# Performance work log

Hardware: AMD Instinct MI355X
Metric: run time of the kernel (lower is better)

Reference implementation:

```python
import jax, jax.numpy as jnp
import numpy as np

D_MODEL, D_K, D_V, H, M = 512, 64, 64, 8, 40
LN_EPS = 1e-3  # keras LayerNormalization default epsilon


def setup_inputs() -> dict:
    key = jax.random.key(0)
    ks = jax.random.split(key, 12)
    b, nq, nk = 16, 1024, 1024
    s = 1.0 / np.sqrt(D_MODEL)
    return {
        "queries": jax.random.normal(ks[0], (b, nq, D_MODEL), jnp.float32),
        "keys": jax.random.normal(ks[1], (b, nk, D_MODEL), jnp.float32),
        "values": jax.random.normal(ks[2], (b, nk, D_MODEL), jnp.float32),
        "attention_weights": jax.random.uniform(ks[3], (b, 1, nq, nk), jnp.float32),
        "Wq": jax.random.normal(ks[4], (D_MODEL, H * D_K), jnp.float32) * s,
        "bq": jnp.zeros((H * D_K,), jnp.float32),
        "Wk": jax.random.normal(ks[5], (D_MODEL, H * D_K), jnp.float32) * s,
        "bk": jnp.zeros((H * D_K,), jnp.float32),
        "Wv": jax.random.normal(ks[6], (D_MODEL, H * D_V), jnp.float32) * s,
        "bv": jnp.zeros((H * D_V,), jnp.float32),
        "Wo": jax.random.normal(ks[7], (H * D_V, D_MODEL), jnp.float32) * (1.0 / np.sqrt(H * D_V)),
        "bo": jnp.zeros((D_MODEL,), jnp.float32),
        "memK": jax.random.normal(ks[8], (1, M, H * D_K), jnp.float32) * (1.0 / D_K),
        "memV": jax.random.normal(ks[9], (1, M, H * D_V), jnp.float32) * (1.0 / M),
        "gamma": jnp.ones((D_MODEL,), jnp.float32),
        "beta": jnp.zeros((D_MODEL,), jnp.float32),
    }


def reference(queries, keys, values, attention_weights, Wq, bq, Wk, bk, Wv, bv,
              Wo, bo, memK, memV, gamma, beta):
    b, nq, _ = queries.shape
    nk = keys.shape[1]
    # scaled learned memory slots
    mem_k = np.sqrt(D_K).astype(np.float32) * memK      # [1, M, H*D_K]
    mem_v = np.sqrt(M).astype(np.float32) * memV        # [1, M, H*D_V]
    # projections
    q = (queries @ Wq + bq).reshape(b, nq, H, D_K).transpose(0, 2, 1, 3)   # [b,h,nq,dk]
    k_proj = keys @ Wk + bk                                                # [b,nk,H*D_K]
    v_proj = values @ Wv + bv                                              # [b,nk,H*D_V]
    k_cat = jnp.concatenate([k_proj, jnp.broadcast_to(mem_k, (b, M, H * D_K))], axis=1)
    v_cat = jnp.concatenate([v_proj, jnp.broadcast_to(mem_v, (b, M, H * D_V))], axis=1)
    k = k_cat.reshape(b, nk + M, H, D_K).transpose(0, 2, 1, 3)             # [b,h,nk+m,dk]
    v = v_cat.reshape(b, nk + M, H, D_V).transpose(0, 2, 1, 3)             # [b,h,nk+m,dv]
    att = jnp.einsum('bhqd,bhkd->bhqk', q, k) / np.sqrt(D_K).astype(np.float32)
    # only the non-memory columns are modulated by attention_weights
    att = jnp.concatenate([att[..., :nk] * attention_weights, att[..., nk:]], axis=-1)
    att = jax.nn.softmax(att, axis=-1)
    out = jnp.einsum('bhqk,bhkd->bhqd', att, v).transpose(0, 2, 1, 3).reshape(b, nq, H * D_V)
    out = out @ Wo + bo  # dropout is identity at inference
    # residual + LayerNorm (keras eps=1e-3)
    x = queries + out
    mu = jnp.mean(x, axis=-1, keepdims=True)
    var = jnp.mean((x - mu) ** 2, axis=-1, keepdims=True)
    return gamma * (x - mu) * jax.lax.rsqrt(var + LN_EPS) + beta
```

## Files before the change

### kernel.cpp

```cpp
#include <hip/hip_runtime.h>
#include <hip/hip_bf16.h>
#include <math.h>

typedef __attribute__((ext_vector_type(8))) short bf16x8;
typedef __attribute__((ext_vector_type(4))) short s16x4;
typedef __attribute__((ext_vector_type(4))) float f32x4;

static __device__ __forceinline__ short f2bf(float f) {
    union { float f; unsigned u; } v; v.f = f;
    unsigned r = v.u + 0x7FFFu + ((v.u >> 16) & 1u);
    return (short)(r >> 16);
}

__global__ __launch_bounds__(256) void wt_kernel(
    const float* __restrict__ Wq, const float* __restrict__ Wk,
    const float* __restrict__ Wv, const float* __restrict__ Wo,
    short* __restrict__ WqT, short* __restrict__ WkT,
    short* __restrict__ WvT, short* __restrict__ WoT)
{
    __shared__ short lds[64][65];
    const float* src; short* dst;
    if (blockIdx.z == 0)      { src = Wq; dst = WqT; }
    else if (blockIdx.z == 1) { src = Wk; dst = WkT; }
    else if (blockIdx.z == 2) { src = Wv; dst = WvT; }
    else                      { src = Wo; dst = WoT; }
    const int kb = blockIdx.x * 64, nb = blockIdx.y * 64;
    const int t = threadIdx.x;
    const int c = t & 63, r0 = t >> 6;
#pragma unroll
    for (int rr = 0; rr < 16; ++rr) {
        const int r = r0 * 16 + rr;
        lds[c][r] = f2bf(src[(size_t)(kb + r) * 512 + nb + c]);
    }
    __syncthreads();
#pragma unroll
    for (int rr = 0; rr < 16; ++rr) {
        const int n = r0 * 16 + rr;
        dst[(size_t)(nb + n) * 512 + kb + c] = lds[n][c];
    }
}

__global__ __launch_bounds__(256) void mem_kernel(
    const float* __restrict__ memK, const float* __restrict__ memV,
    short* __restrict__ Kb, short* __restrict__ VbT)
{
    const int idx = blockIdx.x * 256 + threadIdx.x;
    if (idx >= 16 * 8 * 40 * 64) return;
    const int d = idx & 63;
    const int m = (idx >> 6) % 40;
    const int h = (idx / 2560) & 7;
    const int b = idx / 20480;
    const int src = m * 512 + h * 64 + d;
    const int bh = b * 8 + h;
    Kb[((size_t)bh * 1064 + 1024 + m) * 64 + d] = f2bf(8.0f * memK[src]);
    VbT[((size_t)bh * 64 + d) * 1088 + 1024 + m] = f2bf(sqrtf(40.0f) * memV[src]);
}

__global__ __launch_bounds__(256) void proj_gemm(
    const float* __restrict__ A, const short* __restrict__ BT,
    const float* __restrict__ bias, short* __restrict__ out, int OUTROWS, int vmode)
{
    __shared__ short As[128][40];
    __shared__ short Bs[128][40];
    const int t = threadIdx.x;
    const int lane = t & 63, w = t >> 6;
    const int wr = w >> 1, wc = w & 1;
    const int l16 = lane & 15, g4 = lane >> 4;
    const int m0 = blockIdx.y * 128, n0 = blockIdx.x * 128;

    f32x4 acc[4][4];
#pragma unroll
    for (int i = 0; i < 4; ++i)
#pragma unroll
        for (int j = 0; j < 4; ++j) acc[i][j] = (f32x4){0.f, 0.f, 0.f, 0.f};

    const int sar = t >> 3, sak = (t & 7) * 4;
    const int sbr = t >> 2, sbk = (t & 3) * 8;

    for (int kt = 0; kt < 16; ++kt) {
        const int k0 = kt * 32;
#pragma unroll
        for (int rr = 0; rr < 4; ++rr) {
            const int row = sar + rr * 32;
            const float4 v = *reinterpret_cast<const float4*>(&A[(size_t)(m0 + row) * 512 + k0 + sak]);
            s16x4 bv; bv.x = f2bf(v.x); bv.y = f2bf(v.y); bv.z = f2bf(v.z); bv.w = f2bf(v.w);
            *reinterpret_cast<s16x4*>(&As[row][sak]) = bv;
        }
#pragma unroll
        for (int nn = 0; nn < 2; ++nn) {
            const int nrow = sbr + nn * 64;
            *reinterpret_cast<bf16x8*>(&Bs[nrow][sbk]) =
                *reinterpret_cast<const bf16x8*>(&BT[(size_t)(n0 + nrow) * 512 + k0 + sbk]);
        }
        __syncthreads();
        bf16x8 af[4], bfr[4];
#pragma unroll
        for (int mi = 0; mi < 4; ++mi)
            af[mi] = *reinterpret_cast<const bf16x8*>(&As[wr * 64 + mi * 16 + l16][g4 * 8]);
#pragma unroll
        for (int ni = 0; ni < 4; ++ni)
            bfr[ni] = *reinterpret_cast<const bf16x8*>(&Bs[wc * 64 + ni * 16 + l16][g4 * 8]);
#pragma unroll
        for (int mi = 0; mi < 4; ++mi)
#pragma unroll
            for (int ni = 0; ni < 4; ++ni)
                acc[mi][ni] = __builtin_amdgcn_mfma_f32_16x16x32_bf16(af[mi], bfr[ni], acc[mi][ni], 0, 0, 0);
        __syncthreads();
    }
#pragma unroll
    for (int mi = 0; mi < 4; ++mi) {
#pragma unroll
        for (int ni = 0; ni < 4; ++ni) {
            const int col = n0 + wc * 64 + ni * 16 + l16;
            const int h = col >> 6, d = col & 63;
            const float bb = bias[col];
#pragma unroll
            for (int r = 0; r < 4; ++r) {
                const int rowg = m0 + wr * 64 + mi * 16 + g4 * 4 + r;
                const int b = rowg >> 10, nn = rowg & 1023;
                const short val = f2bf(acc[mi][ni][r] + bb);
                if (vmode)
                    out[(((size_t)b * 8 + h) * 64 + d) * 1088 + nn] = val;
                else
                    out[(((size_t)b * 8 + h) * OUTROWS + nn) * 64 + d] = val;
            }
        }
    }
}

__global__ __launch_bounds__(256) void attn_kernel(
    const short* __restrict__ Qb, const short* __restrict__ Kb,
    const short* __restrict__ VbT, const float* __restrict__ aw,
    short* __restrict__ AO)
{
    __shared__ short Ks[64][72];
    __shared__ short Vs[64][72];
    __shared__ short Ps[4][16][72];

    const int n = blockIdx.x;
    const int xcd = n & 7, s_ = n >> 3, j = s_ & 7, gh = s_ >> 3;
    const int g = gh * 8 + xcd;
    const int h = j, qt = g & 15, b = g >> 4;
    const int bh = b * 8 + h;
    const int t = threadIdx.x;
    const int lane = t & 63, w = t >> 6;
    const int l16 = lane & 15, g4 = lane >> 4;
    const int qrow0 = qt * 64 + w * 16;

    bf16x8 qf0, qf1;
    {
        const short* qp = Qb + ((size_t)bh * 1024 + qrow0 + l16) * 64 + g4 * 8;
        qf0 = *reinterpret_cast<const bf16x8*>(qp);
        qf1 = *reinterpret_cast<const bf16x8*>(qp + 32);
    }

    f32x4 O[4];
#pragma unroll
    for (int i = 0; i < 4; ++i) O[i] = (f32x4){0.f, 0.f, 0.f, 0.f};
    float m_r[4] = {-1e30f, -1e30f, -1e30f, -1e30f};
    float l_r[4] = {0.f, 0.f, 0.f, 0.f};

    const int str = t >> 2;
    const int stc = (t & 3) * 16;

    for (int kt = 0; kt < 17; ++kt) {
        const int kb = kt * 64;
        const bool useaw = (kb < 1024);
        float awv[4][4];
        if (useaw) {
#pragma unroll
            for (int r = 0; r < 4; ++r) {
                const size_t awbase = ((size_t)b * 1024 + qrow0 + g4 * 4 + r) * 1024 + kb + l16;
#pragma unroll
                for (int sub = 0; sub < 4; ++sub)
                    awv[r][sub] = aw[awbase + sub * 16];
            }
        }
        {
            const int rg = kb + str;
            bf16x8 k0 = {0,0,0,0,0,0,0,0}, k1 = {0,0,0,0,0,0,0,0};
            if (rg < 1064) {
                const short* kp = &Kb[((size_t)bh * 1064 + rg) * 64 + stc];
                k0 = *reinterpret_cast<const bf16x8*>(kp);
                k1 = *reinterpret_cast<const bf16x8*>(kp + 8);
            }
            *reinterpret_cast<bf16x8*>(&Ks[str][stc]) = k0;
            *reinterpret_cast<bf16x8*>(&Ks[str][stc + 8]) = k1;
        }
        {
            const short* vp = &VbT[((size_t)bh * 64 + str) * 1088 + kb + stc];
            bf16x8 v0 = {0,0,0,0,0,0,0,0}, v1 = {0,0,0,0,0,0,0,0};
            if (kb + stc + 8 <= 1064)  v0 = *reinterpret_cast<const bf16x8*>(vp);
            if (kb + stc + 16 <= 1064) v1 = *reinterpret_cast<const bf16x8*>(vp + 8);
            *reinterpret_cast<bf16x8*>(&Vs[str][stc]) = v0;
            *reinterpret_cast<bf16x8*>(&Vs[str][stc + 8]) = v1;
        }
        __syncthreads();

        f32x4 S[4];
        __builtin_amdgcn_s_setprio(1);
#pragma unroll
        for (int sub = 0; sub < 4; ++sub) {
            bf16x8 kf0 = *reinterpret_cast<const bf16x8*>(&Ks[sub * 16 + l16][g4 * 8]);
            bf16x8 kf1 = *reinterpret_cast<const bf16x8*>(&Ks[sub * 16 + l16][32 + g4 * 8]);
            f32x4 z = {0.f, 0.f, 0.f, 0.f};
            z = __builtin_amdgcn_mfma_f32_16x16x32_bf16(qf0, kf0, z, 0, 0, 0);
            S[sub] = __builtin_amdgcn_mfma_f32_16x16x32_bf16(qf1, kf1, z, 0, 0, 0);
        }
        __builtin_amdgcn_s_setprio(0);

        const bool tail = (kb + 64 > 1064);
        float corr[4], pv[4][4];
#pragma unroll
        for (int r = 0; r < 4; ++r) {
            float sv[4];
#pragma unroll
            for (int sub = 0; sub < 4; ++sub) {
                float x = S[sub][r] * 0.125f;
                if (useaw) x *= awv[r][sub];
                if (tail && (kb + sub * 16 + l16 >= 1064)) x = -1e30f;
                sv[sub] = x;
            }
            float mx = fmaxf(fmaxf(sv[0], sv[1]), fmaxf(sv[2], sv[3]));
#pragma unroll
            for (int off = 1; off < 16; off <<= 1)
                mx = fmaxf(mx, __shfl_xor(mx, off));
            const float mn = fmaxf(m_r[r], mx);
            corr[r] = __expf(m_r[r] - mn);
            m_r[r] = mn;
            float rs = 0.f;
#pragma unroll
            for (int sub = 0; sub < 4; ++sub) {
                pv[r][sub] = __expf(sv[sub] - mn);
                rs += pv[r][sub];
            }
#pragma unroll
            for (int off = 1; off < 16; off <<= 1)
                rs += __shfl_xor(rs, off);
            l_r[r] = l_r[r] * corr[r] + rs;
        }
#pragma unroll
        for (int r = 0; r < 4; ++r)
#pragma unroll
            for (int sub = 0; sub < 4; ++sub)
                Ps[w][g4 * 4 + r][sub * 16 + l16] = f2bf(pv[r][sub]);
#pragma unroll
        for (int i = 0; i < 4; ++i)
#pragma unroll
            for (int r = 0; r < 4; ++r)
                O[i][r] *= corr[r];
        bf16x8 pf0 = *reinterpret_cast<const bf16x8*>(&Ps[w][l16][g4 * 8]);
        bf16x8 pf1 = *reinterpret_cast<const bf16x8*>(&Ps[w][l16][32 + g4 * 8]);
        __builtin_amdgcn_s_setprio(1);
#pragma unroll
        for (int sub = 0; sub < 4; ++sub) {
            bf16x8 vf0 = *reinterpret_cast<const bf16x8*>(&Vs[sub * 16 + l16][g4 * 8]);
            bf16x8 vf1 = *reinterpret_cast<const bf16x8*>(&Vs[sub * 16 + l16][32 + g4 * 8]);
            O[sub] = __builtin_amdgcn_mfma_f32_16x16x32_bf16(pf0, vf0, O[sub], 0, 0, 0);
            O[sub] = __builtin_amdgcn_mfma_f32_16x16x32_bf16(pf1, vf1, O[sub], 0, 0, 0);
        }
        __builtin_amdgcn_s_setprio(0);
        __syncthreads();
    }
#pragma unroll
    for (int r = 0; r < 4; ++r) {
        const float inv = 1.0f / l_r[r];
        const int qg = qrow0 + g4 * 4 + r;
        const size_t base = ((size_t)b * 1024 + qg) * 512 + h * 64;
#pragma unroll
        for (int sub = 0; sub < 4; ++sub)
            AO[base + sub * 16 + l16] = f2bf(O[sub][r] * inv);
    }
}

__global__ __launch_bounds__(256) void out_gemm(
    const short* __restrict__ A, const short* __restrict__ BT,
    const float* __restrict__ bias, const float* __restrict__ resid,
    float* __restrict__ out)
{
    __shared__ short As[128][40];
    __shared__ short Bs[128][40];
    const int t = threadIdx.x;
    const int lane = t & 63, w = t >> 6;
    const int wr = w >> 1, wc = w & 1;
    const int l16 = lane & 15, g4 = lane >> 4;
    const int m0 = blockIdx.y * 128, n0 = blockIdx.x * 128;

    f32x4 acc[4][4];
#pragma unroll
    for (int i = 0; i < 4; ++i)
#pragma unroll
        for (int j = 0; j < 4; ++j) acc[i][j] = (f32x4){0.f, 0.f, 0.f, 0.f};

    const int sr = t >> 2, sk = (t & 3) * 8;

    for (int kt = 0; kt < 16; ++kt) {
        const int k0 = kt * 32;
#pragma unroll
        for (int nn = 0; nn < 2; ++nn) {
            const int row = sr + nn * 64;
            *reinterpret_cast<bf16x8*>(&As[row][sk]) =
                *reinterpret_cast<const bf16x8*>(&A[(size_t)(m0 + row) * 512 + k0 + sk]);
            *reinterpret_cast<bf16x8*>(&Bs[row][sk]) =
                *reinterpret_cast<const bf16x8*>(&BT[(size_t)(n0 + row) * 512 + k0 + sk]);
        }
        __syncthreads();
        bf16x8 af[4], bfr[4];
#pragma unroll
        for (int mi = 0; mi < 4; ++mi)
            af[mi] = *reinterpret_cast<const bf16x8*>(&As[wr * 64 + mi * 16 + l16][g4 * 8]);
#pragma unroll
        for (int ni = 0; ni < 4; ++ni)
            bfr[ni] = *reinterpret_cast<const bf16x8*>(&Bs[wc * 64 + ni * 16 + l16][g4 * 8]);
#pragma unroll
        for (int mi = 0; mi < 4; ++mi)
#pragma unroll
            for (int ni = 0; ni < 4; ++ni)
                acc[mi][ni] = __builtin_amdgcn_mfma_f32_16x16x32_bf16(af[mi], bfr[ni], acc[mi][ni], 0, 0, 0);
        __syncthreads();
    }
#pragma unroll
    for (int mi = 0; mi < 4; ++mi) {
#pragma unroll
        for (int ni = 0; ni < 4; ++ni) {
            const int col = n0 + wc * 64 + ni * 16 + l16;
            const float bb = bias[col];
#pragma unroll
            for (int r = 0; r < 4; ++r) {
                const int rowg = m0 + wr * 64 + mi * 16 + g4 * 4 + r;
                out[(size_t)rowg * 512 + col] = acc[mi][ni][r] + bb + resid[(size_t)rowg * 512 + col];
            }
        }
    }
}

__global__ __launch_bounds__(256) void ln_kernel(
    float* __restrict__ x, const float* __restrict__ gamma, const float* __restrict__ beta)
{
    const int row = blockIdx.x * 4 + (threadIdx.x >> 6);
    const int lane = threadIdx.x & 63;
    float* rp = x + (size_t)row * 512;
    const float4 v0 = *reinterpret_cast<const float4*>(&rp[lane * 4]);
    const float4 v1 = *reinterpret_cast<const float4*>(&rp[256 + lane * 4]);
    float s = v0.x + v0.y + v0.z + v0.w + v1.x + v1.y + v1.z + v1.w;
    float sq = v0.x * v0.x + v0.y * v0.y + v0.z * v0.z + v0.w * v0.w
             + v1.x * v1.x + v1.y * v1.y + v1.z * v1.z + v1.w * v1.w;
#pragma unroll
    for (int off = 1; off < 64; off <<= 1) {
        s += __shfl_xor(s, off);
        sq += __shfl_xor(sq, off);
    }
    const float mu = s * (1.f / 512.f);
    const float var = sq * (1.f / 512.f) - mu * mu;
    const float inv = rsqrtf(var + 1e-3f);
    const float4 g0 = *reinterpret_cast<const float4*>(&gamma[lane * 4]);
    const float4 g1 = *reinterpret_cast<const float4*>(&gamma[256 + lane * 4]);
    const float4 b0 = *reinterpret_cast<const float4*>(&beta[lane * 4]);
    const float4 b1 = *reinterpret_cast<const float4*>(&beta[256 + lane * 4]);
    float4 o0, o1;
    o0.x = (v0.x - mu) * inv * g0.x + b0.x;
    o0.y = (v0.y - mu) * inv * g0.y + b0.y;
    o0.z = (v0.z - mu) * inv * g0.z + b0.z;
    o0.w = (v0.w - mu) * inv * g0.w + b0.w;
    o1.x = (v1.x - mu) * inv * g1.x + b1.x;
    o1.y = (v1.y - mu) * inv * g1.y + b1.y;
    o1.z = (v1.z - mu) * inv * g1.z + b1.z;
    o1.w = (v1.w - mu) * inv * g1.w + b1.w;
    *reinterpret_cast<float4*>(&rp[lane * 4]) = o0;
    *reinterpret_cast<float4*>(&rp[256 + lane * 4]) = o1;
}

extern "C" void kernel_launch(void* const* d_in, const int* in_sizes, int n_in,
                              void* d_out, int out_size, void* d_ws, size_t ws_size,
                              hipStream_t stream) {
    const float* queries = (const float*)d_in[0];
    const float* keys    = (const float*)d_in[1];
    const float* values  = (const float*)d_in[2];
    const float* aw      = (const float*)d_in[3];
    const float* Wq = (const float*)d_in[4];
    const float* bq = (const float*)d_in[5];
    const float* Wk = (const float*)d_in[6];
    const float* bk = (const float*)d_in[7];
    const float* Wv = (const float*)d_in[8];
    const float* bv = (const float*)d_in[9];
    const float* Wo = (const float*)d_in[10];
    const float* bo = (const float*)d_in[11];
    const float* memK = (const float*)d_in[12];
    const float* memV = (const float*)d_in[13];
    const float* gamma = (const float*)d_in[14];
    const float* beta  = (const float*)d_in[15];
    float* out = (float*)d_out;

    char* ws = (char*)d_ws;
    short* WqT = (short*)(ws + 0);
    short* WkT = (short*)(ws + 524288);
    short* WvT = (short*)(ws + 1048576);
    short* WoT = (short*)(ws + 1572864);
    short* Qb  = (short*)(ws + 2097152);
    short* Kb  = (short*)(ws + 2097152 + 16777216);
    short* VbT = (short*)(ws + 2097152 + 16777216 + 17432576);
    short* AO  = (short*)(ws + 2097152 + 16777216 + 17432576 + 17825792);

    wt_kernel<<<dim3(8, 8, 4), 256, 0, stream>>>(Wq, Wk, Wv, Wo, WqT, WkT, WvT, WoT);
    mem_kernel<<<dim3(1280), 256, 0, stream>>>(memK, memV, Kb, VbT);
    proj_gemm<<<dim3(4, 128), 256, 0, stream>>>(queries, WqT, bq, Qb, 1024, 0);
    proj_gemm<<<dim3(4, 128), 256, 0, stream>>>(keys, WkT, bk, Kb, 1064, 0);
    proj_gemm<<<dim3(4, 128), 256, 0, stream>>>(values, WvT, bv, VbT, 1064, 1);
    attn_kernel<<<dim3(2048), 256, 0, stream>>>(Qb, Kb, VbT, aw, AO);
    out_gemm<<<dim3(4, 128), 256, 0, stream>>>(AO, WoT, bo, queries, out);
    ln_kernel<<<dim3(4096), 256, 0, stream>>>(out, gamma, beta);
}
```

Baseline: 419.0 us.

## Use direct global-to-LDS loads with swizzle in GEMMs and lazy softmax rescaling

The projection and output GEMMs now stage tiles with global_load_lds 16-byte copies into XOR-swizzled LDS, use a 64x128 tile with K-step 64, and double the grid. The projection GEMM keeps fp32 A in LDS and converts to bf16 when building fragments. The attention softmax skips rescaling O and l unless some row max grows by more than 8, and writes P to LDS inside the exp loop. This targets staging overhead, register pressure, bank conflicts and per-tile rescale work, at the cost of a larger fp32 LDS footprint and a threshold-based rescale that allows somewhat larger exponent values.

New measurement: 435.6 us. 1.04x slower.

```diff
diff --git a/kernel.cpp b/kernel.cpp
--- a/kernel.cpp
+++ b/kernel.cpp
@@ -11,6 +11,10 @@
     unsigned r = v.u + 0x7FFFu + ((v.u >> 16) & 1u);
     return (short)(r >> 16);
 }
+
+#define GL2LDS16(g, s) __builtin_amdgcn_global_load_lds( \
+    (const __attribute__((address_space(1))) void*)(g),  \
+    (__attribute__((address_space(3))) void*)(s), 16, 0, 0)
 
 __global__ __launch_bounds__(256) void wt_kernel(
     const float* __restrict__ Wq, const float* __restrict__ Wk,
@@ -60,55 +64,75 @@
     const float* __restrict__ A, const short* __restrict__ BT,
     const float* __restrict__ bias, short* __restrict__ out, int OUTROWS, int vmode)
 {
-    __shared__ short As[128][40];
-    __shared__ short Bs[128][40];
+    __shared__ float As[4096];
+    __shared__ short Bs[8192];
     const int t = threadIdx.x;
     const int lane = t & 63, w = t >> 6;
     const int wr = w >> 1, wc = w & 1;
     const int l16 = lane & 15, g4 = lane >> 4;
-    const int m0 = blockIdx.y * 128, n0 = blockIdx.x * 128;
-
-    f32x4 acc[4][4];
-#pragma unroll
-    for (int i = 0; i < 4; ++i)
+    const int m0 = blockIdx.y * 64, n0 = blockIdx.x * 128;
+
+    f32x4 acc[2][4];
+#pragma unroll
+    for (int i = 0; i < 2; ++i)
 #pragma unroll
         for (int j = 0; j < 4; ++j) acc[i][j] = (f32x4){0.f, 0.f, 0.f, 0.f};
 
-    const int sar = t >> 3, sak = (t & 7) * 4;
-    const int sbr = t >> 2, sbk = (t & 3) * 8;
-
-    for (int kt = 0; kt < 16; ++kt) {
-        const int k0 = kt * 32;
-#pragma unroll
-        for (int rr = 0; rr < 4; ++rr) {
-            const int row = sar + rr * 32;
-            const float4 v = *reinterpret_cast<const float4*>(&A[(size_t)(m0 + row) * 512 + k0 + sak]);
-            s16x4 bv; bv.x = f2bf(v.x); bv.y = f2bf(v.y); bv.z = f2bf(v.z); bv.w = f2bf(v.w);
-            *reinterpret_cast<s16x4*>(&As[row][sak]) = bv;
-        }
-#pragma unroll
-        for (int nn = 0; nn < 2; ++nn) {
-            const int nrow = sbr + nn * 64;
-            *reinterpret_cast<bf16x8*>(&Bs[nrow][sbk]) =
-                *reinterpret_cast<const bf16x8*>(&BT[(size_t)(n0 + nrow) * 512 + k0 + sbk]);
-        }
-        __syncthreads();
-        bf16x8 af[4], bfr[4];
-#pragma unroll
-        for (int mi = 0; mi < 4; ++mi)
-            af[mi] = *reinterpret_cast<const bf16x8*>(&As[wr * 64 + mi * 16 + l16][g4 * 8]);
-#pragma unroll
-        for (int ni = 0; ni < 4; ++ni)
-            bfr[ni] = *reinterpret_cast<const bf16x8*>(&Bs[wc * 64 + ni * 16 + l16][g4 * 8]);
-#pragma unroll
-        for (int mi = 0; mi < 4; ++mi)
-#pragma unroll
-            for (int ni = 0; ni < 4; ++ni)
-                acc[mi][ni] = __builtin_amdgcn_mfma_f32_16x16x32_bf16(af[mi], bfr[ni], acc[mi][ni], 0, 0, 0);
-        __syncthreads();
-    }
-#pragma unroll
-    for (int mi = 0; mi < 4; ++mi) {
+    int arow_[4], acol_[4], brow_[4], bcol_[4];
+#pragma unroll
+    for (int c = 0; c < 4; ++c) {
+        const int chunk = c * 4 + w;
+        const int ar = chunk * 4 + (lane >> 4);
+        const int alb = ((lane & 15) * 16) ^ ((ar & 7) << 4);
+        arow_[c] = ar; acol_[c] = alb >> 2;
+        const int br = chunk * 8 + (lane >> 3);
+        const int blb = ((lane & 7) * 16) ^ ((br & 7) << 4);
+        brow_[c] = br; bcol_[c] = blb >> 1;
+    }
+
+    for (int kt = 0; kt < 8; ++kt) {
+        const int k0 = kt * 64;
+#pragma unroll
+        for (int c = 0; c < 4; ++c) {
+            GL2LDS16(&A[(size_t)(m0 + arow_[c]) * 512 + k0 + acol_[c]],
+                     &As[(c * 4 + w) * 256 + lane * 4]);
+            GL2LDS16(&BT[(size_t)(n0 + brow_[c]) * 512 + k0 + bcol_[c]],
+                     &Bs[(c * 4 + w) * 512 + lane * 8]);
+        }
+        __syncthreads();
+#pragma unroll
+        for (int kk = 0; kk < 2; ++kk) {
+            bf16x8 af[2], bfr[4];
+#pragma unroll
+            for (int mi = 0; mi < 2; ++mi) {
+                const int ar = wr * 32 + mi * 16 + l16;
+                const int lb0 = (kk * 128 + g4 * 32) ^ ((ar & 7) << 4);
+                const float4 f0 = *reinterpret_cast<const float4*>(
+                    reinterpret_cast<const char*>(As) + ar * 256 + lb0);
+                const float4 f1 = *reinterpret_cast<const float4*>(
+                    reinterpret_cast<const char*>(As) + ar * 256 + (lb0 ^ 16));
+                bf16x8 a;
+                a[0] = f2bf(f0.x); a[1] = f2bf(f0.y); a[2] = f2bf(f0.z); a[3] = f2bf(f0.w);
+                a[4] = f2bf(f1.x); a[5] = f2bf(f1.y); a[6] = f2bf(f1.z); a[7] = f2bf(f1.w);
+                af[mi] = a;
+            }
+#pragma unroll
+            for (int ni = 0; ni < 4; ++ni) {
+                const int br = wc * 64 + ni * 16 + l16;
+                const int lb = (kk * 64 + g4 * 16) ^ ((br & 7) << 4);
+                bfr[ni] = *reinterpret_cast<const bf16x8*>(
+                    reinterpret_cast<const char*>(Bs) + br * 128 + lb);
+            }
+#pragma unroll
+            for (int mi = 0; mi < 2; ++mi)
+#pragma unroll
+                for (int ni = 0; ni < 4; ++ni)
+                    acc[mi][ni] = __builtin_amdgcn_mfma_f32_16x16x32_bf16(af[mi], bfr[ni], acc[mi][ni], 0, 0, 0);
+        }
+        __syncthreads();
+    }
+#pragma unroll
+    for (int mi = 0; mi < 2; ++mi) {
 #pragma unroll
         for (int ni = 0; ni < 4; ++ni) {
             const int col = n0 + wc * 64 + ni * 16 + l16;
@@ -116,7 +140,7 @@
             const float bb = bias[col];
 #pragma unroll
             for (int r = 0; r < 4; ++r) {
-                const int rowg = m0 + wr * 64 + mi * 16 + g4 * 4 + r;
+                const int rowg = m0 + wr * 32 + mi * 16 + g4 * 4 + r;
                 const int b = rowg >> 10, nn = rowg & 1023;
                 const short val = f2bf(acc[mi][ni][r] + bb);
                 if (vmode)
@@ -210,45 +234,50 @@
         __builtin_amdgcn_s_setprio(0);
 
         const bool tail = (kb + 64 > 1064);
-        float corr[4], pv[4][4];
+        float sv[4][4], mx[4];
 #pragma unroll
         for (int r = 0; r < 4; ++r) {
-            float sv[4];
 #pragma unroll
             for (int sub = 0; sub < 4; ++sub) {
                 float x = S[sub][r] * 0.125f;
                 if (useaw) x *= awv[r][sub];
                 if (tail && (kb + sub * 16 + l16 >= 1064)) x = -1e30f;
-                sv[sub] = x;
-            }
-            float mx = fmaxf(fmaxf(sv[0], sv[1]), fmaxf(sv[2], sv[3]));
+                sv[r][sub] = x;
+            }
+            float m2 = fmaxf(fmaxf(sv[r][0], sv[r][1]), fmaxf(sv[r][2], sv[r][3]));
 #pragma unroll
             for (int off = 1; off < 16; off <<= 1)
-                mx = fmaxf(mx, __shfl_xor(mx, off));
-            const float mn = fmaxf(m_r[r], mx);
-            corr[r] = __expf(m_r[r] - mn);
-            m_r[r] = mn;
+                m2 = fmaxf(m2, __shfl_xor(m2, off));
+            mx[r] = m2;
+        }
+        bool grew = false;
+#pragma unroll
+        for (int r = 0; r < 4; ++r) grew = grew || (mx[r] > m_r[r] + 8.0f);
+        if (__any(grew)) {
+#pragma unroll
+            for (int r = 0; r < 4; ++r) {
+                const float mn = fmaxf(m_r[r], mx[r]);
+                const float corr = __expf(m_r[r] - mn);
+                m_r[r] = mn;
+                l_r[r] *= corr;
+#pragma unroll
+                for (int i = 0; i < 4; ++i) O[i][r] *= corr;
+            }
+        }
+#pragma unroll
+        for (int r = 0; r < 4; ++r) {
             float rs = 0.f;
 #pragma unroll
             for (int sub = 0; sub < 4; ++sub) {
-                pv[r][sub] = __expf(sv[sub] - mn);
-                rs += pv[r][sub];
+                const float p = __expf(sv[r][sub] - m_r[r]);
+                rs += p;
+                Ps[w][g4 * 4 + r][sub * 16 + l16] = f2bf(p);
             }
 #pragma unroll
             for (int off = 1; off < 16; off <<= 1)
                 rs += __shfl_xor(rs, off);
-            l_r[r] = l_r[r] * corr[r] + rs;
-        }
-#pragma unroll
-        for (int r = 0; r < 4; ++r)
-#pragma unroll
-            for (int sub = 0; sub < 4; ++sub)
-                Ps[w][g4 * 4 + r][sub * 16 + l16] = f2bf(pv[r][sub]);
-#pragma unroll
-        for (int i = 0; i < 4; ++i)
-#pragma unroll
-            for (int r = 0; r < 4; ++r)
-                O[i][r] *= corr[r];
+            l_r[r] += rs;
+        }
         bf16x8 pf0 = *reinterpret_cast<const bf16x8*>(&Ps[w][l16][g4 * 8]);
         bf16x8 pf1 = *reinterpret_cast<const bf16x8*>(&Ps[w][l16][32 + g4 * 8]);
         __builtin_amdgcn_s_setprio(1);
@@ -278,56 +307,81 @@
     const float* __restrict__ bias, const float* __restrict__ resid,
     float* __restrict__ out)
 {
-    __shared__ short As[128][40];
-    __shared__ short Bs[128][40];
+    __shared__ short Asb[4096];
+    __shared__ short Bs[8192];
     const int t = threadIdx.x;
     const int lane = t & 63, w = t >> 6;
     const int wr = w >> 1, wc = w & 1;
     const int l16 = lane & 15, g4 = lane >> 4;
-    const int m0 = blockIdx.y * 128, n0 = blockIdx.x * 128;
-
-    f32x4 acc[4][4];
-#pragma unroll
-    for (int i = 0; i < 4; ++i)
+    const int m0 = blockIdx.y * 64, n0 = blockIdx.x * 128;
+
+    f32x4 acc[2][4];
+#pragma unroll
+    for (int i = 0; i < 2; ++i)
 #pragma unroll
         for (int j = 0; j < 4; ++j) acc[i][j] = (f32x4){0.f, 0.f, 0.f, 0.f};
 
-    const int sr = t >> 2, sk = (t & 3) * 8;
-
-    for (int kt = 0; kt < 16; ++kt) {
-        const int k0 = kt * 32;
-#pragma unroll
-        for (int nn = 0; nn < 2; ++nn) {
-            const int row = sr + nn * 64;
-            *reinterpret_cast<bf16x8*>(&As[row][sk]) =
-                *reinterpret_cast<const bf16x8*>(&A[(size_t)(m0 + row) * 512 + k0 + sk]);
-            *reinterpret_cast<bf16x8*>(&Bs[row][sk]) =
-                *reinterpret_cast<const bf16x8*>(&BT[(size_t)(n0 + row) * 512 + k0 + sk]);
-        }
-        __syncthreads();
-        bf16x8 af[4], bfr[4];
-#pragma unroll
-        for (int mi = 0; mi < 4; ++mi)
-            af[mi] = *reinterpret_cast<const bf16x8*>(&As[wr * 64 + mi * 16 + l16][g4 * 8]);
-#pragma unroll
-        for (int ni = 0; ni < 4; ++ni)
-            bfr[ni] = *reinterpret_cast<const bf16x8*>(&Bs[wc * 64 + ni * 16 + l16][g4 * 8]);
-#pragma unroll
-        for (int mi = 0; mi < 4; ++mi)
-#pragma unroll
-            for (int ni = 0; ni < 4; ++ni)
-                acc[mi][ni] = __builtin_amdgcn_mfma_f32_16x16x32_bf16(af[mi], bfr[ni], acc[mi][ni], 0, 0, 0);
-        __syncthreads();
-    }
-#pragma unroll
-    for (int mi = 0; mi < 4; ++mi) {
+    int arow_[2], acol_[2], brow_[4], bcol_[4];
+#pragma unroll
+    for (int c = 0; c < 2; ++c) {
+        const int chunk = c * 4 + w;
+        const int ar = chunk * 8 + (lane >> 3);
+        const int alb = ((lane & 7) * 16) ^ ((ar & 7) << 4);
+        arow_[c] = ar; acol_[c] = alb >> 1;
+    }
+#pragma unroll
+    for (int c = 0; c < 4; ++c) {
+        const int chunk = c * 4 + w;
+        const int br = chunk * 8 + (lane >> 3);
+        const int blb = ((lane & 7) * 16) ^ ((br & 7) << 4);
+        brow_[c] = br; bcol_[c] = blb >> 1;
+    }
+
+    for (int kt = 0; kt < 8; ++kt) {
+        const int k0 = kt * 64;
+#pragma unroll
+        for (int c = 0; c < 2; ++c)
+            GL2LDS16(&A[(size_t)(m0 + arow_[c]) * 512 + k0 + acol_[c]],
+                     &Asb[(c * 4 + w) * 512 + lane * 8]);
+#pragma unroll
+        for (int c = 0; c < 4; ++c)
+            GL2LDS16(&BT[(size_t)(n0 + brow_[c]) * 512 + k0 + bcol_[c]],
+                     &Bs[(c * 4 + w) * 512 + lane * 8]);
+        __syncthreads();
+#pragma unroll
+        for (int kk = 0; kk < 2; ++kk) {
+            bf16x8 af[2], bfr[4];
+#pragma unroll
+            for (int mi = 0; mi < 2; ++mi) {
+                const int ar = wr * 32 + mi * 16 + l16;
+                const int lb = (kk * 64 + g4 * 16) ^ ((ar & 7) << 4);
+                af[mi] = *reinterpret_cast<const bf16x8*>(
+                    reinterpret_cast<const char*>(Asb) + ar * 128 + lb);
+            }
+#pragma unroll
+            for (int ni = 0; ni < 4; ++ni) {
+                const int br = wc * 64 + ni * 16 + l16;
+                const int lb = (kk * 64 + g4 * 16) ^ ((br & 7) << 4);
+                bfr[ni] = *reinterpret_cast<const bf16x8*>(
+                    reinterpret_cast<const char*>(Bs) + br * 128 + lb);
+            }
+#pragma unroll
+            for (int mi = 0; mi < 2; ++mi)
+#pragma unroll
+                for (int ni = 0; ni < 4; ++ni)
+                    acc[mi][ni] = __builtin_amdgcn_mfma_f32_16x16x32_bf16(af[mi], bfr[ni], acc[mi][ni], 0, 0, 0);
+        }
+        __syncthreads();
+    }
+#pragma unroll
+    for (int mi = 0; mi < 2; ++mi) {
 #pragma unroll
         for (int ni = 0; ni < 4; ++ni) {
             const int col = n0 + wc * 64 + ni * 16 + l16;
             const float bb = bias[col];
 #pragma unroll
             for (int r = 0; r < 4; ++r) {
-                const int rowg = m0 + wr * 64 + mi * 16 + g4 * 4 + r;
+                const int rowg = m0 + wr * 32 + mi * 16 + g4 * 4 + r;
                 out[(size_t)rowg * 512 + col] = acc[mi][ni][r] + bb + resid[(size_t)rowg * 512 + col];
             }
         }
@@ -403,10 +457,10 @@
 
     wt_kernel<<<dim3(8, 8, 4), 256, 0, stream>>>(Wq, Wk, Wv, Wo, WqT, WkT, WvT, WoT);
     mem_kernel<<<dim3(1280), 256, 0, stream>>>(memK, memV, Kb, VbT);
-    proj_gemm<<<dim3(4, 128), 256, 0, stream>>>(queries, WqT, bq, Qb, 1024, 0);
-    proj_gemm<<<dim3(4, 128), 256, 0, stream>>>(keys, WkT, bk, Kb, 1064, 0);
-    proj_gemm<<<dim3(4, 128), 256, 0, stream>>>(values, WvT, bv, VbT, 1064, 1);
+    proj_gemm<<<dim3(4, 256), 256, 0, stream>>>(queries, WqT, bq, Qb, 1024, 0);
+    proj_gemm<<<dim3(4, 256), 256, 0, stream>>>(keys, WkT, bk, Kb, 1064, 0);
+    proj_gemm<<<dim3(4, 256), 256, 0, stream>>>(values, WvT, bv, VbT, 1064, 1);
     attn_kernel<<<dim3(2048), 256, 0, stream>>>(Qb, Kb, VbT, aw, AO);
-    out_gemm<<<dim3(4, 128), 256, 0, stream>>>(AO, WoT, bo, queries, out);
+    out_gemm<<<dim3(4, 256), 256, 0, stream>>>(AO, WoT, bo, queries, out);
     ln_kernel<<<dim3(4096), 256, 0, stream>>>(out, gamma, beta);
 }
```
